# Performance work log

Hardware: AMD Instinct MI355X
Metric: run time of the kernel (lower is better)

Reference implementation:

```python
import jax, jax.numpy as jnp
import numpy as np

S = 4096
DMODEL = 1024
DK = 128

def setup_inputs() -> dict:
    key = jax.random.key(0)
    ks = jax.random.split(key, 7)
    X = jax.random.normal(ks[0], (S, DMODEL), dtype=jnp.float32)
    # nn.Linear(dmodel, dk): weight [dk, dmodel], bias [dk]
    sc = 1.0 / np.sqrt(DMODEL)
    Wq = jax.random.uniform(ks[1], (DK, DMODEL), jnp.float32, -sc, sc)
    bq = jax.random.uniform(ks[2], (DK,), jnp.float32, -sc, sc)
    Wk = jax.random.uniform(ks[3], (DK, DMODEL), jnp.float32, -sc, sc)
    bk = jax.random.uniform(ks[4], (DK,), jnp.float32, -sc, sc)
    Wv = jax.random.uniform(ks[5], (DK, DMODEL), jnp.float32, -sc, sc)
    bv = jax.random.uniform(ks[6], (DK,), jnp.float32, -sc, sc)
    return {"X": X, "Wq": Wq, "bq": bq, "Wk": Wk, "bk": bk, "Wv": Wv, "bv": bv}

def reference(X, Wq, bq, Wk, bk, Wv, bv):
    # QKV projections: [S, dk]
    Q = X @ Wq.T + bq
    K = X @ Wk.T + bk
    V = X @ Wv.T + bv
    scale = 1.0 / jnp.sqrt(jnp.asarray(DK, X.dtype))
    scores = (Q @ K.T) * scale  # [S, S]
    s = X.shape[0]
    causal = jnp.tril(jnp.ones((s, s), dtype=bool))  # True = keep
    scores = jnp.where(causal, scores, -jnp.inf)
    A = jax.nn.softmax(scores, axis=-1)  # dropout p=0 -> identity
    return A @ V  # [S, dk]
```

## Files before the change

kernel.cpp:

```cpp
#include <hip/hip_runtime.h>
#include <hip/hip_bf16.h>

#define S 4096
#define DMODEL 1024
#define DK 128
#define NB_ATTN 528

typedef __attribute__((ext_vector_type(8))) short  short8;
typedef __attribute__((ext_vector_type(4))) float  f32x4;
typedef __attribute__((ext_vector_type(4))) unsigned short u16x4;

__device__ __forceinline__ unsigned short f2bf(float f) {
    return __builtin_bit_cast(unsigned short, __float2bfloat16(f));
}

__device__ __forceinline__ short8 cvt8(float4 a, float4 b) {
    short8 v;
    v[0] = (short)f2bf(a.x); v[1] = (short)f2bf(a.y);
    v[2] = (short)f2bf(a.z); v[3] = (short)f2bf(a.w);
    v[4] = (short)f2bf(b.x); v[5] = (short)f2bf(b.y);
    v[6] = (short)f2bf(b.z); v[7] = (short)f2bf(b.w);
    return v;
}

__global__ __launch_bounds__(256) void cvt_kernel(
    const float* __restrict__ X,
    const float* __restrict__ Wq, const float* __restrict__ Wk,
    const float* __restrict__ Wv,
    unsigned short* __restrict__ Xb, unsigned short* __restrict__ Wb)
{
    const int i = blockIdx.x * 256 + threadIdx.x;
    const float* __restrict__ src;
    unsigned short* __restrict__ dst;
    size_t off;
    if (i < 524288) {
        src = X; dst = Xb; off = (size_t)i * 8;
    } else {
        const int j   = i - 524288;
        const int sel = j >> 14, jj = j & 16383;
        src = sel == 0 ? Wq : sel == 1 ? Wk : Wv;
        dst = Wb + (size_t)sel * DK * DMODEL;
        off = (size_t)jj * 8;
    }
    const float4 a = *(const float4*)(src + off);
    const float4 b = *(const float4*)(src + off + 4);
    *(short8*)(dst + off) = cvt8(a, b);
}

__global__ __launch_bounds__(128) void proj_gemm(
    const unsigned short* __restrict__ Xb, const unsigned short* __restrict__ Wb,
    const float* __restrict__ bq, const float* __restrict__ bk,
    const float* __restrict__ bv,
    unsigned short* __restrict__ Qb, unsigned short* __restrict__ Kb,
    unsigned short* __restrict__ Vt)
{
    const int sel = blockIdx.y;
    const float* __restrict__ bias = sel == 0 ? bq : sel == 1 ? bk : bv;
    const unsigned short* __restrict__ wbase = Wb + (size_t)sel * DK * DMODEL;

    const int tid = threadIdx.x, w = tid >> 6, lane = tid & 63;
    const int li = lane & 15, gl = lane >> 4;
    const int r0 = blockIdx.x * 16;
    const int n0 = blockIdx.z * 64 + w * 32;

    f32x4 acc[2];
    #pragma unroll
    for (int j = 0; j < 2; ++j)
        #pragma unroll
        for (int r = 0; r < 4; ++r) acc[j][r] = 0.f;

    const unsigned short* ap  = &Xb[(size_t)(r0 + li) * DMODEL + 8 * gl];
    const unsigned short* bp0 = &wbase[(size_t)(n0 + li) * DMODEL + 8 * gl];
    const unsigned short* bp1 = bp0 + (size_t)16 * DMODEL;

    #pragma unroll 4
    for (int k0 = 0; k0 < DMODEL; k0 += 32) {
        const short8 a  = *(const short8*)(ap + k0);
        const short8 b0 = *(const short8*)(bp0 + k0);
        const short8 b1 = *(const short8*)(bp1 + k0);
        acc[0] = __builtin_amdgcn_mfma_f32_16x16x32_bf16(a, b0, acc[0], 0, 0, 0);
        acc[1] = __builtin_amdgcn_mfma_f32_16x16x32_bf16(a, b1, acc[1], 0, 0, 0);
    }

    if (sel < 2) {
        unsigned short* __restrict__ Out = sel == 0 ? Qb : Kb;
        #pragma unroll
        for (int j = 0; j < 2; ++j)
            #pragma unroll
            for (int r = 0; r < 4; ++r) {
                const int row = r0 + 4 * gl + r;
                const int col = n0 + 16 * j + li;
                Out[(size_t)row * DK + col] = f2bf(acc[j][r] + bias[col]);
            }
    } else {
        #pragma unroll
        for (int j = 0; j < 2; ++j) {
            const int col = n0 + 16 * j + li;
            const float bb = bias[col];
            u16x4 wv;
            #pragma unroll
            for (int r = 0; r < 4; ++r) wv[r] = f2bf(acc[j][r] + bb);
            *(u16x4*)&Vt[(size_t)col * S + r0 + 4 * gl] = wv;
        }
    }
}

__global__ __launch_bounds__(256, 2) void attn_mfma(
    const unsigned short* __restrict__ Qb,
    const unsigned short* __restrict__ Kb,
    const unsigned short* __restrict__ Vt,
    float* __restrict__ OP, float* __restrict__ ML)
{
    const int bb = blockIdx.x;
    int T = 0;
    while ((T + 1) * (T + 2) / 2 <= bb) ++T;
    const int c = bb - T * (T + 1) / 2;
    const int kstart = 128 * c;

    const int tid = threadIdx.x, w = tid >> 6, lane = tid & 63;
    const int li = lane & 15, gl = lane >> 4;
    const int q0 = 128 * T + 32 * w;

    __shared__ unsigned short Ks[2][32 * DK];
    __shared__ unsigned short Vs[2][DK * 32];
    __shared__ unsigned short Pl[4][32][40];

    short8 aq[2][4];
    #pragma unroll
    for (int qs = 0; qs < 2; ++qs)
        #pragma unroll
        for (int s = 0; s < 4; ++s)
            aq[qs][s] = *(const short8*)
                &Qb[(size_t)(q0 + 16 * qs + li) * DK + 32 * s + 8 * gl];

    f32x4 accv[2][8];
    #pragma unroll
    for (int qs = 0; qs < 2; ++qs)
        #pragma unroll
        for (int n = 0; n < 8; ++n)
            #pragma unroll
            for (int r = 0; r < 4; ++r) accv[qs][n][r] = 0.f;

    float mr[2] = {-1e30f, -1e30f}, lr[2] = {0.f, 0.f};
    const float scale = 0.08838834764831845f;

    {
        short8 st0 = *(const short8*)&Kb[(size_t)(kstart + (tid >> 4)) * DK + (tid & 15) * 8];
        short8 st1 = *(const short8*)&Kb[(size_t)(kstart + (tid >> 4) + 16) * DK + (tid & 15) * 8];
        short8 st2 = *(const short8*)&Vt[(size_t)(tid >> 2) * S + kstart + (tid & 3) * 8];
        short8 st3 = *(const short8*)&Vt[(size_t)((tid >> 2) + 64) * S + kstart + (tid & 3) * 8];
        *(short8*)&Ks[0][(size_t)tid * 8]         = st0;
        *(short8*)&Ks[0][(size_t)(tid + 256) * 8] = st1;
        *(short8*)&Vs[0][(size_t)tid * 8]         = st2;
        *(short8*)&Vs[0][(size_t)(tid + 256) * 8] = st3;
    }
    __syncthreads();

    int cur = 0;
    for (int it = 0; it < 4; ++it) {
        const int kb = kstart + 32 * it;
        const bool pf = (it < 3);

        short8 st0, st1, st2, st3;
        if (pf) {
            const int kn = kb + 32;
            st0 = *(const short8*)&Kb[(size_t)(kn + (tid >> 4)) * DK + (tid & 15) * 8];
            st1 = *(const short8*)&Kb[(size_t)(kn + (tid >> 4) + 16) * DK + (tid & 15) * 8];
            st2 = *(const short8*)&Vt[(size_t)(tid >> 2) * S + kn + (tid & 3) * 8];
            st3 = *(const short8*)&Vt[(size_t)((tid >> 2) + 64) * S + kn + (tid & 3) * 8];
        }

        const unsigned short* Ksb = &Ks[cur][0];
        const unsigned short* Vsb = &Vs[cur][0];
        short8 kf[2][4], vf[8];
        #pragma unroll
        for (int kt = 0; kt < 2; ++kt)
            #pragma unroll
            for (int s = 0; s < 4; ++s)
                kf[kt][s] = *(const short8*)&Ksb[(16 * kt + li) * DK + 32 * s + 8 * gl];
        #pragma unroll
        for (int n = 0; n < 8; ++n)
            vf[n] = *(const short8*)&Vsb[(16 * n + li) * 32 + 8 * gl];

        f32x4 sc[2][2];
        #pragma unroll
        for (int qs = 0; qs < 2; ++qs)
            #pragma unroll
            for (int kt = 0; kt < 2; ++kt)
                #pragma unroll
                for (int r = 0; r < 4; ++r) sc[qs][kt][r] = 0.f;
        __builtin_amdgcn_s_setprio(1);
        #pragma unroll
        for (int qs = 0; qs < 2; ++qs)
            #pragma unroll
            for (int kt = 0; kt < 2; ++kt)
                #pragma unroll
                for (int s = 0; s < 4; ++s)
                    sc[qs][kt] = __builtin_amdgcn_mfma_f32_16x16x32_bf16(
                        kf[kt][s], aq[qs][s], sc[qs][kt], 0, 0, 0);
        __builtin_amdgcn_s_setprio(0);

        #pragma unroll
        for (int qs = 0; qs < 2; ++qs) {
            const int q = q0 + 16 * qs + li;
            #pragma unroll
            for (int kt = 0; kt < 2; ++kt)
                #pragma unroll
                for (int r = 0; r < 4; ++r) {
                    const int key = kb + 16 * kt + 4 * gl + r;
                    sc[qs][kt][r] = (key > q) ? -1e30f : sc[qs][kt][r] * scale;
                }
        }

        float tm[2];
        #pragma unroll
        for (int qs = 0; qs < 2; ++qs) {
            float v = fmaxf(fmaxf(fmaxf(sc[qs][0][0], sc[qs][0][1]),
                                  fmaxf(sc[qs][0][2], sc[qs][0][3])),
                            fmaxf(fmaxf(sc[qs][1][0], sc[qs][1][1]),
                                  fmaxf(sc[qs][1][2], sc[qs][1][3])));
            v = fmaxf(v, __shfl_xor(v, 16));
            v = fmaxf(v, __shfl_xor(v, 32));
            tm[qs] = v;
        }

        const int need = (tm[0] > mr[0] + 6.f) | (tm[1] > mr[1] + 6.f);
        if (__any(need)) {
            float corr[2];
            #pragma unroll
            for (int qs = 0; qs < 2; ++qs) {
                const float mnew = fmaxf(mr[qs], tm[qs]);
                corr[qs] = __expf(mr[qs] - mnew);
                lr[qs] *= corr[qs];
                mr[qs]  = mnew;
            }
            #pragma unroll
            for (int qs = 0; qs < 2; ++qs)
                #pragma unroll
                for (int r = 0; r < 4; ++r) {
                    const float cr = __shfl(corr[qs], 4 * gl + r);
                    #pragma unroll
                    for (int n = 0; n < 8; ++n) accv[qs][n][r] *= cr;
                }
        }

        #pragma unroll
        for (int qs = 0; qs < 2; ++qs) {
            float ps = 0.f;
            #pragma unroll
            for (int kt = 0; kt < 2; ++kt)
                #pragma unroll
                for (int r = 0; r < 4; ++r) {
                    const float p = __expf(sc[qs][kt][r] - mr[qs]);
                    sc[qs][kt][r] = p;
                    ps += p;
                }
            ps += __shfl_xor(ps, 16);
            ps += __shfl_xor(ps, 32);
            lr[qs] += ps;
        }

        #pragma unroll
        for (int qs = 0; qs < 2; ++qs)
            #pragma unroll
            for (int kt = 0; kt < 2; ++kt) {
                u16x4 wv;
                #pragma unroll
                for (int r = 0; r < 4; ++r) wv[r] = f2bf(sc[qs][kt][r]);
                *(u16x4*)&Pl[w][16 * qs + li][16 * kt + 4 * gl] = wv;
            }
        const short8 pa0 = *(const short8*)&Pl[w][li][8 * gl];
        const short8 pa1 = *(const short8*)&Pl[w][16 + li][8 * gl];

        __builtin_amdgcn_s_setprio(1);
        #pragma unroll
        for (int n = 0; n < 8; ++n) {
            accv[0][n] = __builtin_amdgcn_mfma_f32_16x16x32_bf16(pa0, vf[n], accv[0][n], 0, 0, 0);
            accv[1][n] = __builtin_amdgcn_mfma_f32_16x16x32_bf16(pa1, vf[n], accv[1][n], 0, 0, 0);
        }
        __builtin_amdgcn_s_setprio(0);

        if (pf) {
            *(short8*)&Ks[cur ^ 1][(size_t)tid * 8]         = st0;
            *(short8*)&Ks[cur ^ 1][(size_t)(tid + 256) * 8] = st1;
            *(short8*)&Vs[cur ^ 1][(size_t)tid * 8]         = st2;
            *(short8*)&Vs[cur ^ 1][(size_t)(tid + 256) * 8] = st3;
            __syncthreads();
        }
        cur ^= 1;
    }

    #pragma unroll
    for (int qs = 0; qs < 2; ++qs)
        #pragma unroll
        for (int n = 0; n < 8; ++n)
            #pragma unroll
            for (int r = 0; r < 4; ++r)
                __builtin_nontemporal_store(accv[qs][n][r],
                    &OP[((size_t)bb * 128 + 32 * w + 16 * qs + 4 * gl + r) * DK
                        + 16 * n + li]);
    if (gl == 0) {
        #pragma unroll
        for (int qs = 0; qs < 2; ++qs) {
            ML[((size_t)bb * 128 + 32 * w + 16 * qs + li) * 2 + 0] = mr[qs];
            ML[((size_t)bb * 128 + 32 * w + 16 * qs + li) * 2 + 1] = lr[qs];
        }
    }
}

__global__ __launch_bounds__(DK) void merge_kernel(
    const float* __restrict__ OP, const float* __restrict__ ML,
    float* __restrict__ out)
{
    const int row = blockIdx.x, dv = threadIdx.x;
    const int T  = row >> 7, rl = row & 127;
    const int j  = T + 1;
    const int base = T * (T + 1) / 2;

    float M = -1e30f;
    for (int c = 0; c < j; ++c)
        M = fmaxf(M, ML[((size_t)(base + c) * 128 + rl) * 2]);
    float L = 0.f, o = 0.f;
    #pragma unroll 2
    for (int c = 0; c < j; ++c) {
        const float mc = ML[((size_t)(base + c) * 128 + rl) * 2 + 0];
        const float lc = ML[((size_t)(base + c) * 128 + rl) * 2 + 1];
        const float wgt = __expf(mc - M);
        L += lc * wgt;
        o += wgt * __builtin_nontemporal_load(
                 &OP[((size_t)(base + c) * 128 + rl) * DK + dv]);
    }
    out[(size_t)row * DK + dv] = o / L;
}

extern "C" void kernel_launch(void* const* d_in, const int* in_sizes, int n_in,
                              void* d_out, int out_size, void* d_ws, size_t ws_size,
                              hipStream_t stream)
{
    (void)in_sizes; (void)n_in; (void)out_size; (void)ws_size;
    const float* X  = (const float*)d_in[0];
    const float* Wq = (const float*)d_in[1];
    const float* bq = (const float*)d_in[2];
    const float* Wk = (const float*)d_in[3];
    const float* bk = (const float*)d_in[4];
    const float* Wv = (const float*)d_in[5];
    const float* bv = (const float*)d_in[6];
    float* out = (float*)d_out;

    unsigned short* Wb = (unsigned short*)d_ws;
    unsigned short* Qb = Wb + (size_t)3 * DK * DMODEL;
    unsigned short* Kb = Qb + (size_t)S * DK;
    unsigned short* Vt = Kb + (size_t)S * DK;
    unsigned short* Xb = Vt + (size_t)S * DK;
    float* OP = (float*)Xb;
    float* ML = OP + (size_t)NB_ATTN * 128 * DK;

    cvt_kernel<<<2240, 256, 0, stream>>>(X, Wq, Wk, Wv, Xb, Wb);
    proj_gemm<<<dim3(S / 16, 3, 2), 128, 0, stream>>>(
        Xb, Wb, bq, bk, bv, Qb, Kb, Vt);
    attn_mfma<<<NB_ATTN, 256, 0, stream>>>(Qb, Kb, Vt, OP, ML);
    merge_kernel<<<S, DK, 0, stream>>>(OP, ML, out);
}
```

Measured before the change: 147.0 us.

## Halve attention query tile to 64 rows, trim causal key range, swizzle LDS

The attention kernel now uses 128-thread blocks covering 64 query rows each, with a new triangular block-index mapping over 128-key chunks. Each block's key loop stops at the causal diagonal instead of always running four 32-key steps. K and V tiles are written to shared memory with an XOR swizzle to avoid bank conflicts. The merge kernel is reindexed for the new partial layout and reads (m,l) pairs as float2. Twice as many blocks with fewer warps each raises parallelism and skips masked work, at the cost of more K/V traffic and more partials to merge.

Result: slower. 150.9 us (+2.7%).

```diff
diff --git a/kernel.cpp b/kernel.cpp
--- a/kernel.cpp
+++ b/kernel.cpp
@@ -4,7 +4,7 @@
 #define S 4096
 #define DMODEL 1024
 #define DK 128
-#define NB_ATTN 528
+#define NB_ATTN 1056
 
 typedef __attribute__((ext_vector_type(8))) short  short8;
 typedef __attribute__((ext_vector_type(4))) float  f32x4;
@@ -105,25 +105,28 @@
     }
 }
 
-__global__ __launch_bounds__(256, 2) void attn_mfma(
+__global__ __launch_bounds__(128) void attn_mfma(
     const unsigned short* __restrict__ Qb,
     const unsigned short* __restrict__ Kb,
     const unsigned short* __restrict__ Vt,
     float* __restrict__ OP, float* __restrict__ ML)
 {
     const int bb = blockIdx.x;
-    int T = 0;
-    while ((T + 1) * (T + 2) / 2 <= bb) ++T;
-    const int c = bb - T * (T + 1) / 2;
+    int m = 0;
+    while ((m + 1) * (m + 2) <= bb) ++m;
+    const int r_ = bb - m * (m + 1);
+    const int t  = (r_ < m + 1) ? 2 * m : 2 * m + 1;
+    const int c  = (r_ < m + 1) ? r_ : r_ - (m + 1);
     const int kstart = 128 * c;
+    const int kend   = min(128 * (c + 1), 64 * t + 64);
 
     const int tid = threadIdx.x, w = tid >> 6, lane = tid & 63;
     const int li = lane & 15, gl = lane >> 4;
-    const int q0 = 128 * T + 32 * w;
+    const int q0 = 64 * t + 32 * w;
 
     __shared__ unsigned short Ks[2][32 * DK];
     __shared__ unsigned short Vs[2][DK * 32];
-    __shared__ unsigned short Pl[4][32][40];
+    __shared__ unsigned short Pl[2][32][40];
 
     short8 aq[2][4];
     #pragma unroll
@@ -145,29 +148,36 @@
     const float scale = 0.08838834764831845f;
 
     {
-        short8 st0 = *(const short8*)&Kb[(size_t)(kstart + (tid >> 4)) * DK + (tid & 15) * 8];
-        short8 st1 = *(const short8*)&Kb[(size_t)(kstart + (tid >> 4) + 16) * DK + (tid & 15) * 8];
-        short8 st2 = *(const short8*)&Vt[(size_t)(tid >> 2) * S + kstart + (tid & 3) * 8];
-        short8 st3 = *(const short8*)&Vt[(size_t)((tid >> 2) + 64) * S + kstart + (tid & 3) * 8];
-        *(short8*)&Ks[0][(size_t)tid * 8]         = st0;
-        *(short8*)&Ks[0][(size_t)(tid + 256) * 8] = st1;
-        *(short8*)&Vs[0][(size_t)tid * 8]         = st2;
-        *(short8*)&Vs[0][(size_t)(tid + 256) * 8] = st3;
+        #pragma unroll
+        for (int i = 0; i < 4; ++i) {
+            const int ch = tid + 128 * i;
+            const int key = ch >> 4, ckk = ch & 15;
+            const int dv  = ch >> 2, ckv = ch & 3;
+            const short8 sk = *(const short8*)
+                &Kb[(size_t)(kstart + key) * DK + ckk * 8];
+            const short8 sv = *(const short8*)
+                &Vt[(size_t)dv * S + kstart + ckv * 8];
+            *(short8*)&Ks[0][key * DK + ((ckk ^ (key & 7)) * 8)] = sk;
+            *(short8*)&Vs[0][dv * 32 + ((ckv ^ ((dv >> 1) & 3)) * 8)] = sv;
+        }
     }
     __syncthreads();
 
     int cur = 0;
-    for (int it = 0; it < 4; ++it) {
-        const int kb = kstart + 32 * it;
-        const bool pf = (it < 3);
-
-        short8 st0, st1, st2, st3;
+    for (int kb = kstart; kb < kend; kb += 32) {
+        const bool pf = (kb + 32 < kend);
+
+        short8 stK[4], stV[4];
         if (pf) {
             const int kn = kb + 32;
-            st0 = *(const short8*)&Kb[(size_t)(kn + (tid >> 4)) * DK + (tid & 15) * 8];
-            st1 = *(const short8*)&Kb[(size_t)(kn + (tid >> 4) + 16) * DK + (tid & 15) * 8];
-            st2 = *(const short8*)&Vt[(size_t)(tid >> 2) * S + kn + (tid & 3) * 8];
-            st3 = *(const short8*)&Vt[(size_t)((tid >> 2) + 64) * S + kn + (tid & 3) * 8];
+            #pragma unroll
+            for (int i = 0; i < 4; ++i) {
+                const int ch = tid + 128 * i;
+                stK[i] = *(const short8*)
+                    &Kb[(size_t)(kn + (ch >> 4)) * DK + (ch & 15) * 8];
+                stV[i] = *(const short8*)
+                    &Vt[(size_t)(ch >> 2) * S + kn + (ch & 3) * 8];
+            }
         }
 
         const unsigned short* Ksb = &Ks[cur][0];
@@ -177,10 +187,12 @@
         for (int kt = 0; kt < 2; ++kt)
             #pragma unroll
             for (int s = 0; s < 4; ++s)
-                kf[kt][s] = *(const short8*)&Ksb[(16 * kt + li) * DK + 32 * s + 8 * gl];
+                kf[kt][s] = *(const short8*)
+                    &Ksb[(16 * kt + li) * DK + (((4 * s + gl) ^ (li & 7)) * 8)];
         #pragma unroll
         for (int n = 0; n < 8; ++n)
-            vf[n] = *(const short8*)&Vsb[(16 * n + li) * 32 + 8 * gl];
+            vf[n] = *(const short8*)
+                &Vsb[(16 * n + li) * 32 + ((gl ^ ((li >> 1) & 3)) * 8)];
 
         f32x4 sc[2][2];
         #pragma unroll
@@ -281,10 +293,14 @@
         __builtin_amdgcn_s_setprio(0);
 
         if (pf) {
-            *(short8*)&Ks[cur ^ 1][(size_t)tid * 8]         = st0;
-            *(short8*)&Ks[cur ^ 1][(size_t)(tid + 256) * 8] = st1;
-            *(short8*)&Vs[cur ^ 1][(size_t)tid * 8]         = st2;
-            *(short8*)&Vs[cur ^ 1][(size_t)(tid + 256) * 8] = st3;
+            #pragma unroll
+            for (int i = 0; i < 4; ++i) {
+                const int ch = tid + 128 * i;
+                const int key = ch >> 4, ckk = ch & 15;
+                const int dv  = ch >> 2, ckv = ch & 3;
+                *(short8*)&Ks[cur ^ 1][key * DK + ((ckk ^ (key & 7)) * 8)] = stK[i];
+                *(short8*)&Vs[cur ^ 1][dv * 32 + ((ckv ^ ((dv >> 1) & 3)) * 8)] = stV[i];
+            }
             __syncthreads();
         }
         cur ^= 1;
@@ -297,13 +313,13 @@
             #pragma unroll
             for (int r = 0; r < 4; ++r)
                 __builtin_nontemporal_store(accv[qs][n][r],
-                    &OP[((size_t)bb * 128 + 32 * w + 16 * qs + 4 * gl + r) * DK
+                    &OP[((size_t)bb * 64 + 32 * w + 16 * qs + 4 * gl + r) * DK
                         + 16 * n + li]);
     if (gl == 0) {
         #pragma unroll
         for (int qs = 0; qs < 2; ++qs) {
-            ML[((size_t)bb * 128 + 32 * w + 16 * qs + li) * 2 + 0] = mr[qs];
-            ML[((size_t)bb * 128 + 32 * w + 16 * qs + li) * 2 + 1] = lr[qs];
+            ML[((size_t)bb * 64 + 32 * w + 16 * qs + li) * 2 + 0] = mr[qs];
+            ML[((size_t)bb * 64 + 32 * w + 16 * qs + li) * 2 + 1] = lr[qs];
         }
     }
 }
@@ -313,22 +329,22 @@
     float* __restrict__ out)
 {
     const int row = blockIdx.x, dv = threadIdx.x;
-    const int T  = row >> 7, rl = row & 127;
-    const int j  = T + 1;
-    const int base = T * (T + 1) / 2;
+    const int T  = row >> 6, rl = row & 63;
+    const int m  = T >> 1;
+    const int j  = m + 1;
+    const int base = (T & 1) ? (m + 1) * (m + 1) : m * (m + 1);
 
     float M = -1e30f;
     for (int c = 0; c < j; ++c)
-        M = fmaxf(M, ML[((size_t)(base + c) * 128 + rl) * 2]);
+        M = fmaxf(M, ((const float2*)ML)[(size_t)(base + c) * 64 + rl].x);
     float L = 0.f, o = 0.f;
     #pragma unroll 2
     for (int c = 0; c < j; ++c) {
-        const float mc = ML[((size_t)(base + c) * 128 + rl) * 2 + 0];
-        const float lc = ML[((size_t)(base + c) * 128 + rl) * 2 + 1];
-        const float wgt = __expf(mc - M);
-        L += lc * wgt;
+        const float2 ml = ((const float2*)ML)[(size_t)(base + c) * 64 + rl];
+        const float wgt = __expf(ml.x - M);
+        L += ml.y * wgt;
         o += wgt * __builtin_nontemporal_load(
-                 &OP[((size_t)(base + c) * 128 + rl) * DK + dv]);
+                 &OP[((size_t)(base + c) * 64 + rl) * DK + dv]);
     }
     out[(size_t)row * DK + dv] = o / L;
 }
@@ -353,11 +369,11 @@
     unsigned short* Vt = Kb + (size_t)S * DK;
     unsigned short* Xb = Vt + (size_t)S * DK;
     float* OP = (float*)Xb;
-    float* ML = OP + (size_t)NB_ATTN * 128 * DK;
+    float* ML = OP + (size_t)NB_ATTN * 64 * DK;
 
     cvt_kernel<<<2240, 256, 0, stream>>>(X, Wq, Wk, Wv, Xb, Wb);
     proj_gemm<<<dim3(S / 16, 3, 2), 128, 0, stream>>>(
         Xb, Wb, bq, bk, bv, Qb, Kb, Vt);
-    attn_mfma<<<NB_ATTN, 256, 0, stream>>>(Qb, Kb, Vt, OP, ML);
+    attn_mfma<<<NB_ATTN, 128, 0, stream>>>(Qb, Kb, Vt, OP, ML);
     merge_kernel<<<S, DK, 0, stream>>>(OP, ML, out);
 }
```
